# Kernel tuning notes

Hardware: AMD Instinct MI355X
Metric: run time of the kernel (lower is better)

The kernel has to match this reference:

```python
import jax, jax.numpy as jnp
import numpy as np
import math

DIM, DEPTH, HEADS, DH, MLP = 512, 12, 8, 64, 2048
EPS = 1e-5

def _ln(x, g, b):
    m = jnp.mean(x, -1, keepdims=True)
    v = jnp.var(x, -1, keepdims=True)
    return (x - m) * jax.lax.rsqrt(v + EPS) * g + b

def _gelu(x):
    return jax.nn.gelu(x, approximate=False)  # torch nn.GELU default = exact erf

def _conv1d(x, w, b):
    # x: [B, Cin, T], w: [Cout, Cin, 7], 'same' padding
    y = jax.lax.conv_general_dilated(x, w, (1,), [(3, 3)], dimension_numbers=('NCH', 'OIH', 'NCH'))
    return y + b[None, :, None]

def setup_inputs() -> dict:
    key = jax.random.key(0)
    ks = iter(jax.random.split(key, 64))
    def w(shape, s=0.02):
        return jax.random.normal(next(ks), shape, jnp.float32) * s
    return {
        'x': jax.random.normal(next(ks), (2, 1024), jnp.float32),
        'timesteps': jax.random.uniform(next(ks), (2,), jnp.float32) * 1000.0,
        'cond': jax.random.normal(next(ks), (2, 64, DIM), jnp.float32),
        'conv_w1': w((DIM // 2, 1, 7)), 'conv_b1': jnp.zeros((DIM // 2,), jnp.float32),
        'conv_w2': w((DIM, DIM // 2, 7)), 'conv_b2': jnp.zeros((DIM,), jnp.float32),
        'tpe_w1': w((DIM, 4 * DIM)), 'tpe_b1': jnp.zeros((4 * DIM,), jnp.float32),
        'tpe_w2': w((4 * DIM, DIM)), 'tpe_b2': jnp.zeros((DIM,), jnp.float32),
        'ln1_g': jnp.ones((DEPTH, DIM), jnp.float32), 'ln1_b': jnp.zeros((DEPTH, DIM), jnp.float32),
        'wq': w((DEPTH, DIM, HEADS * DH)), 'wkv': w((DEPTH, DIM, 2 * DH)),
        'wo': w((DEPTH, HEADS * DH, DIM)), 'bo': jnp.zeros((DEPTH, DIM), jnp.float32),
        'ln2_g': jnp.ones((DEPTH, DIM), jnp.float32), 'ln2_b': jnp.zeros((DEPTH, DIM), jnp.float32),
        'ffn_w1': w((DEPTH, DIM, MLP)), 'ffn_b1': jnp.zeros((DEPTH, MLP), jnp.float32),
        'ffn_w2': w((DEPTH, MLP, DIM)), 'ffn_b2': jnp.zeros((DEPTH, DIM), jnp.float32),
        'tm_w1': w((DEPTH, DIM, 4 * DIM)), 'tm_b1': jnp.zeros((DEPTH, 4 * DIM), jnp.float32),
        'tm_w2': w((DEPTH, 4 * DIM, DIM)), 'tm_b2': jnp.zeros((DEPTH, DIM), jnp.float32),
        'fn_g': jnp.ones((DIM,), jnp.float32), 'fn_b': jnp.zeros((DIM,), jnp.float32),
        'out_w1': w((DIM, 2 * DIM)), 'out_b1': jnp.zeros((2 * DIM,), jnp.float32),
        'out_w2': w((2 * DIM, 1)), 'out_b2': jnp.zeros((1,), jnp.float32),
    }

def reference(x, timesteps, cond, conv_w1, conv_b1, conv_w2, conv_b2,
              tpe_w1, tpe_b1, tpe_w2, tpe_b2,
              ln1_g, ln1_b, wq, wkv, wo, bo, ln2_g, ln2_b,
              ffn_w1, ffn_b1, ffn_w2, ffn_b2, tm_w1, tm_b1, tm_w2, tm_b2,
              fn_g, fn_b, out_w1, out_b1, out_w2, out_b2):
    b, T = x.shape
    # audio encoder: conv -> relu -> conv -> relu
    h = _conv1d(x[:, None, :], conv_w1, conv_b1)
    h = jax.nn.relu(h)
    h = _conv1d(h, conv_w2, conv_b2)
    h = jax.nn.relu(h)
    h = h.transpose(0, 2, 1)  # [b, T, dim]
    # sinusoidal time embedding + MLP
    half = DIM // 2
    freqs = jnp.exp(jnp.arange(half, dtype=jnp.float32) * (-math.log(10000.0) / (half - 1)))
    te = timesteps[:, None] * freqs[None, :]
    te = jnp.concatenate([jnp.sin(te), jnp.cos(te)], axis=-1)  # [b, dim]
    time_emb = _gelu(te @ tpe_w1 + tpe_b1) @ tpe_w2 + tpe_b2
    # concat text conditioning tokens
    h = jnp.concatenate([h, cond], axis=1)  # [b, n, dim]
    bsz, n, _ = h.shape
    scale = DH ** -0.5

    def block(hx, p):
        g1, b1, Wq, Wkv, Wo, Bo, g2, b2, F1, Fb1, F2, Fb2, T1, Tb1, T2, Tb2 = p
        tm = _gelu(time_emb @ T1 + Tb1) @ T2 + Tb2  # [b, dim]
        hx = _ln(hx, g1, b1)
        q = (hx @ Wq).reshape(bsz, n, HEADS, DH).transpose(0, 2, 1, 3)  # [b,h,n,d]
        kv = hx @ Wkv
        k, v = kv[..., :DH], kv[..., DH:]  # shared single KV head [b,n,d]
        dots = jnp.einsum('bhnd,bmd->bhnm', q, k) * scale
        attn = jax.nn.softmax(dots, axis=-1)
        o = jnp.einsum('bhnm,bmd->bhnd', attn, v)
        o = o.transpose(0, 2, 1, 3).reshape(bsz, n, HEADS * DH) @ Wo + Bo
        hx = hx + o
        hx = hx + tm[:, None, :]
        hx = _ln(hx, g2, b2)
        hx = hx + (_gelu(hx @ F1 + Fb1) @ F2 + Fb2)
        return hx, None

    h, _ = jax.lax.scan(block, h, (ln1_g, ln1_b, wq, wkv, wo, bo, ln2_g, ln2_b,
                                   ffn_w1, ffn_b1, ffn_w2, ffn_b2,
                                   tm_w1, tm_b1, tm_w2, tm_b2))
    h = _ln(h, fn_g, fn_b)
    h = _gelu(h @ out_w1 + out_b1) @ out_w2 + out_b2  # [b, n, 1]
    return h[:, :T, 0]
```

## Files before the change

kernel.cpp:

```cpp
#include <hip/hip_runtime.h>
#include <hip/hip_bf16.h>
#include <math.h>


typedef unsigned short u16;
typedef __attribute__((ext_vector_type(8))) short short8;
typedef __attribute__((ext_vector_type(8))) unsigned short ushort8;
typedef __attribute__((ext_vector_type(4))) float f32x4;

#define MFMA_B16(a, b, c) __builtin_amdgcn_mfma_f32_16x16x32_bf16(a, b, c, 0, 0, 0)

__device__ __forceinline__ float gelu_f(float x) {
  return 0.5f * x * (1.f + erff(x * 0.70710678118654752f));
}
__device__ __forceinline__ u16 f2b(float x) {
  union { float f; unsigned u; } v;
  v.f = x;
  unsigned r = (v.u + 0x7FFF + ((v.u >> 16) & 1)) >> 16;
  return (u16)r;
}
__device__ __forceinline__ float b2f(u16 u) {
  union { unsigned u; float f; } v;
  v.u = ((unsigned)u) << 16;
  return v.f;
}

#define MODE_BIAS 1
#define MODE_GELU 2
#define MODE_RES 4
#define MODE_TM 8
#define MODE_OUT16 16
#define MODE_KVT 32
#define MODE_RELU 64
#define MODE_CONVROW 128

__global__ void te_k(const float* __restrict__ ts, float* __restrict__ te) {
  int t = threadIdx.x;
  int b = t >> 8, i = t & 255;
  float tv = ts[b];
  float fr = __expf((float)i * (-9.210340371976184f / 255.f));
  float arg = tv * fr;
  te[b * 512 + i] = sinf(arg);
  te[b * 512 + 256 + i] = cosf(arg);
}

__global__ __launch_bounds__(256) void mlpA_k(const float* __restrict__ A,
                                              const float* __restrict__ B,
                                              float* __restrict__ part, int K,
                                              int N, long sA, long sB) {
  int l = blockIdx.z;
  const float* Ap = A + (size_t)l * sA;
  const float* Bp = B + (size_t)l * sB;
  int KS = K >> 7;
  int tid = threadIdx.x;
  int c16 = tid & 15;
  int col = blockIdx.x * 64 + c16 * 4;
  int kr = tid >> 4;
  int k0 = blockIdx.y * 128 + kr;
  float4 a0 = {0.f, 0.f, 0.f, 0.f}, a1 = {0.f, 0.f, 0.f, 0.f};
#pragma unroll
  for (int i = 0; i < 8; ++i) {
    int k = k0 + i * 16;
    float4 bv = *(const float4*)&Bp[(size_t)k * N + col];
    float x0 = Ap[k], x1 = Ap[K + k];
    a0.x = fmaf(x0, bv.x, a0.x);
    a0.y = fmaf(x0, bv.y, a0.y);
    a0.z = fmaf(x0, bv.z, a0.z);
    a0.w = fmaf(x0, bv.w, a0.w);
    a1.x = fmaf(x1, bv.x, a1.x);
    a1.y = fmaf(x1, bv.y, a1.y);
    a1.z = fmaf(x1, bv.z, a1.z);
    a1.w = fmaf(x1, bv.w, a1.w);
  }
#pragma unroll
  for (int off = 16; off < 64; off <<= 1) {
    a0.x += __shfl_xor(a0.x, off);
    a0.y += __shfl_xor(a0.y, off);
    a0.z += __shfl_xor(a0.z, off);
    a0.w += __shfl_xor(a0.w, off);
    a1.x += __shfl_xor(a1.x, off);
    a1.y += __shfl_xor(a1.y, off);
    a1.z += __shfl_xor(a1.z, off);
    a1.w += __shfl_xor(a1.w, off);
  }
  __shared__ float red[4][2][64];
  int w = tid >> 6, lane = tid & 63;
  if (lane < 16) {
    *(float4*)&red[w][0][c16 * 4] = a0;
    *(float4*)&red[w][1][c16 * 4] = a1;
  }
  __syncthreads();
  if (tid < 128) {
    int m = tid >> 6, c = tid & 63;
    float s = red[0][m][c] + red[1][m][c] + red[2][m][c] + red[3][m][c];
    part[(((size_t)l * KS + blockIdx.y) * 2 + m) * N + blockIdx.x * 64 + c] = s;
  }
}

__global__ __launch_bounds__(256) void mlpB_k(const float* __restrict__ part,
                                              const float* __restrict__ bias,
                                              float* __restrict__ C, int N,
                                              int lgN, int KS, int dogelu,
                                              long sb, long sC) {
  int idx = blockIdx.x * 256 + threadIdx.x;
  int col = idx & (N - 1);
  int lm = idx >> lgN;
  int m = lm & 1, l = lm >> 1;
  float s = 0.f;
  for (int ks = 0; ks < KS; ++ks)
    s += part[(((size_t)l * KS + ks) * 2 + m) * N + col];
  s += bias[(size_t)l * sb + col];
  if (dogelu) s = gelu_f(s);
  C[(size_t)l * sC + (size_t)m * N + col] = s;
}

__global__ __launch_bounds__(256) void conv1_k(const float* __restrict__ x,
                                               const float* __restrict__ w1,
                                               const float* __restrict__ b1,
                                               float* __restrict__ buf1) {
  int idx = blockIdx.x * 256 + threadIdx.x;
  int t = idx & 1023, co = (idx >> 10) & 255, b = idx >> 18;
  float acc = b1[co];
#pragma unroll
  for (int k = 0; k < 7; ++k) {
    int gt = t + k - 3;
    if (gt >= 0 && gt < 1024)
      acc = fmaf(w1[co * 7 + k], x[b * 1024 + gt], acc);
  }
  buf1[idx] = fmaxf(acc, 0.f);
}

__global__ __launch_bounds__(256) void im2col_k(const float* __restrict__ buf1,
                                                u16* __restrict__ A16) {
  int idx = blockIdx.x * 256 + threadIdx.x;
  int c = idx % 1792;
  int m = idx / 1792;
  int b = m >> 10, tt = m & 1023;
  int ci = c / 7, k = c - ci * 7;
  int gt = tt + k - 3;
  float v = (gt >= 0 && gt < 1024) ? buf1[((b * 256) + ci) * 1024 + gt] : 0.f;
  A16[idx] = f2b(v);
}

__global__ void cond_k(const float* __restrict__ cond,
                       float* __restrict__ hbuf) {
  int idx = blockIdx.x * 256 + threadIdx.x;
  int b = idx >> 15, rem = idx & 32767;
  int j = rem >> 9, cc = rem & 511;
  hbuf[(size_t)(b * 1088 + 1024 + j) * 512 + cc] = cond[idx];
}

__global__ __launch_bounds__(256) void ln_k(float* __restrict__ h,
                                            u16* __restrict__ h16,
                                            const float* __restrict__ g,
                                            const float* __restrict__ bb) {
  int row = blockIdx.x;
  float* p = h + (size_t)row * 512;
  int t = threadIdx.x;
  float x0 = p[t], x1 = p[t + 256];
  float s = x0 + x1, q = x0 * x0 + x1 * x1;
#pragma unroll
  for (int off = 1; off < 64; off <<= 1) {
    s += __shfl_xor(s, off);
    q += __shfl_xor(q, off);
  }
  __shared__ float ps[4], pq[4];
  int w = t >> 6, lane = t & 63;
  if (lane == 0) {
    ps[w] = s;
    pq[w] = q;
  }
  __syncthreads();
  s = ps[0] + ps[1] + ps[2] + ps[3];
  q = pq[0] + pq[1] + pq[2] + pq[3];
  float mean = s * (1.f / 512.f);
  float var = q * (1.f / 512.f) - mean * mean;
  float rs = rsqrtf(var + 1e-5f);
  float v0 = (x0 - mean) * rs * g[t] + bb[t];
  float v1 = (x1 - mean) * rs * g[t + 256] + bb[t + 256];
  p[t] = v0;
  p[t + 256] = v1;
  h16[(size_t)row * 512 + t] = f2b(v0);
  h16[(size_t)row * 512 + t + 256] = f2b(v1);
}

__device__ __forceinline__ void wcvt_tile(float (*T)[65],
                                          const float* __restrict__ src,
                                          u16* __restrict__ dst, int K, int N,
                                          int tk, int tn, int t) {
  int kl = t >> 2, nseg = (t & 3) * 16;
#pragma unroll
  for (int j = 0; j < 4; ++j) {
    float4 v =
        *(const float4*)&src[(size_t)(tk * 64 + kl) * N + tn * 64 + nseg + j * 4];
    T[nseg + j * 4 + 0][kl] = v.x;
    T[nseg + j * 4 + 1][kl] = v.y;
    T[nseg + j * 4 + 2][kl] = v.z;
    T[nseg + j * 4 + 3][kl] = v.w;
  }
  __syncthreads();
  int nl = t >> 2, kseg = (t & 3) * 16;
#pragma unroll
  for (int j = 0; j < 4; ++j) {
    ushort4 o;
    o.x = f2b(T[nl][kseg + j * 4 + 0]);
    o.y = f2b(T[nl][kseg + j * 4 + 1]);
    o.z = f2b(T[nl][kseg + j * 4 + 2]);
    o.w = f2b(T[nl][kseg + j * 4 + 3]);
    *(ushort4*)&dst[(size_t)(tn * 64 + nl) * K + tk * 64 + kseg + j * 4] = o;
  }
}

__global__ __launch_bounds__(256) void wcvt5_k(
    const float* wq, const float* wkv, const float* wo, const float* w1,
    const float* w2, u16* dq, u16* dkv, u16* dwo, u16* d1, u16* d2) {
  __shared__ float T[64][65];
  int bid = blockIdx.x, t = threadIdx.x;
  if (bid < 64) {
    wcvt_tile(T, wq, dq, 512, 512, bid >> 3, bid & 7, t);
  } else if (bid < 80) {
    int id = bid - 64;
    wcvt_tile(T, wkv, dkv, 512, 128, id >> 1, id & 1, t);
  } else if (bid < 144) {
    int id = bid - 80;
    wcvt_tile(T, wo, dwo, 512, 512, id >> 3, id & 7, t);
  } else if (bid < 400) {
    int id = bid - 144;
    wcvt_tile(T, w1, d1, 512, 2048, id >> 5, id & 31, t);
  } else {
    int id = bid - 400;
    wcvt_tile(T, w2, d2, 2048, 512, id >> 3, id & 7, t);
  }
}

__global__ __launch_bounds__(256) void wcvtT_k(const float* src, u16* dst,
                                               int K, int N) {
  __shared__ float T[64][65];
  int nt = N >> 6;
  int tk = blockIdx.x / nt, tn = blockIdx.x % nt;
  wcvt_tile(T, src, dst, K, N, tk, tn, threadIdx.x);
}

__global__ __launch_bounds__(256) void fcvt_k(const float* __restrict__ src,
                                              u16* __restrict__ dst, int n) {
  int i = (blockIdx.x * 256 + threadIdx.x) * 4;
  if (i >= n) return;
  float4 v = *(const float4*)&src[i];
  ushort4 o;
  o.x = f2b(v.x);
  o.y = f2b(v.y);
  o.z = f2b(v.z);
  o.w = f2b(v.w);
  *(ushort4*)&dst[i] = o;
}

__global__ __launch_bounds__(256) void bgemm2_k(
    const u16* __restrict__ A, const u16* __restrict__ B,
    const float* __restrict__ bias, const float* __restrict__ tmv,
    const float* __restrict__ res, float* __restrict__ Cf,
    u16* __restrict__ C16, u16* __restrict__ C16b, float* __restrict__ part,
    int K, int N, int Kblk, int MN, int mode) {
  __shared__ u16 As[2][64 * 72];
  __shared__ u16 Bs[2][64 * 72];
  int t = threadIdx.x;
  int n0 = blockIdx.x * 64, m0 = blockIdx.y * 64;
  int kz = blockIdx.z;
  int wid = t >> 6, lane = t & 63;
  int quad = lane >> 4, l15 = lane & 15;
  int wr = (wid >> 1) * 32, wc = (wid & 1) * 32;
  int sr = t >> 2, sc = (t & 3) * 16;
  const u16* Ap = A + (size_t)(m0 + sr) * K + (size_t)kz * Kblk + sc;
  const u16* Bp = B + (size_t)(n0 + sr) * K + (size_t)kz * Kblk + sc;

  f32x4 acc[2][2];
#pragma unroll
  for (int i = 0; i < 2; ++i)
#pragma unroll
    for (int j = 0; j < 2; ++j) acc[i][j] = (f32x4){0.f, 0.f, 0.f, 0.f};

  int nt = Kblk >> 6;
  ushort8 ra0 = *(const ushort8*)Ap;
  ushort8 ra1 = *(const ushort8*)(Ap + 8);
  ushort8 rb0 = *(const ushort8*)Bp;
  ushort8 rb1 = *(const ushort8*)(Bp + 8);
  *(ushort8*)&As[0][sr * 72 + sc] = ra0;
  *(ushort8*)&As[0][sr * 72 + sc + 8] = ra1;
  *(ushort8*)&Bs[0][sr * 72 + sc] = rb0;
  *(ushort8*)&Bs[0][sr * 72 + sc + 8] = rb1;
  __syncthreads();
  int cur = 0;
  for (int tt = 0; tt < nt; ++tt) {
    if (tt + 1 < nt) {
      const u16* ap = Ap + (tt + 1) * 64;
      const u16* bp = Bp + (tt + 1) * 64;
      ra0 = *(const ushort8*)ap;
      ra1 = *(const ushort8*)(ap + 8);
      rb0 = *(const ushort8*)bp;
      rb1 = *(const ushort8*)(bp + 8);
    }
    short8 af[2][2], bf[2][2];
#pragma unroll
    for (int s = 0; s < 2; ++s)
#pragma unroll
      for (int i = 0; i < 2; ++i) {
        af[i][s] =
            *(const short8*)&As[cur][(wr + i * 16 + l15) * 72 + s * 32 + quad * 8];
        bf[i][s] =
            *(const short8*)&Bs[cur][(wc + i * 16 + l15) * 72 + s * 32 + quad * 8];
      }
#pragma unroll
    for (int s = 0; s < 2; ++s)
#pragma unroll
      for (int i = 0; i < 2; ++i)
#pragma unroll
        for (int j = 0; j < 2; ++j)
          acc[i][j] = MFMA_B16(af[i][s], bf[j][s], acc[i][j]);
    if (tt + 1 < nt) {
      int nx = cur ^ 1;
      *(ushort8*)&As[nx][sr * 72 + sc] = ra0;
      *(ushort8*)&As[nx][sr * 72 + sc + 8] = ra1;
      *(ushort8*)&Bs[nx][sr * 72 + sc] = rb0;
      *(ushort8*)&Bs[nx][sr * 72 + sc + 8] = rb1;
      __syncthreads();
      cur = nx;
    }
  }

  if (gridDim.z > 1) {
#pragma unroll
    for (int i = 0; i < 2; ++i)
#pragma unroll
      for (int reg = 0; reg < 4; ++reg) {
        int row = m0 + wr + i * 16 + quad * 4 + reg;
#pragma unroll
        for (int j = 0; j < 2; ++j) {
          int col = n0 + wc + j * 16 + l15;
          part[(size_t)kz * MN + (size_t)row * N + col] = acc[i][j][reg];
        }
      }
    return;
  }

#pragma unroll
  for (int i = 0; i < 2; ++i) {
#pragma unroll
    for (int reg = 0; reg < 4; ++reg) {
      int row = m0 + wr + i * 16 + quad * 4 + reg;
      int orow = (mode & MODE_CONVROW) ? row + ((row >> 10) << 6) : row;
#pragma unroll
      for (int j = 0; j < 2; ++j) {
        int col = n0 + wc + j * 16 + l15;
        float v = acc[i][j][reg];
        if (mode & MODE_BIAS) v += bias[col];
        if (mode & MODE_TM) v += tmv[(row >= 1088 ? 512 : 0) + col];
        if (mode & MODE_RES) v += res[(size_t)orow * 512 + col];
        if (mode & MODE_GELU) v = gelu_f(v);
        if (mode & MODE_RELU) v = fmaxf(v, 0.f);
        if (mode & MODE_KVT) {
          if (col < 64)
            C16[orow * 64 + col] = f2b(v);
          else
            C16b[(size_t)(col - 64) * 2176 + orow] = f2b(v);
        } else if (mode & MODE_OUT16) {
          C16[(size_t)orow * N + col] = f2b(v);
        } else {
          Cf[(size_t)orow * N + col] = v;
        }
      }
    }
  }
}

__global__ __launch_bounds__(256) void bred_k(
    const float* __restrict__ part, const float* __restrict__ bias,
    const float* __restrict__ tmv, const float* __restrict__ res,
    float* __restrict__ Cf, u16* __restrict__ C16, u16* __restrict__ C16b,
    int MN, int Nmask, int lgN, int S, int mode) {
  int idx = (blockIdx.x * 256 + threadIdx.x) * 4;
  if (idx >= MN) return;
  int row = idx >> lgN;
  int col = idx & Nmask;
  float4 s = *(const float4*)&part[idx];
  for (int ss = 1; ss < S; ++ss) {
    float4 p = *(const float4*)&part[(size_t)ss * MN + idx];
    s.x += p.x;
    s.y += p.y;
    s.z += p.z;
    s.w += p.w;
  }
  float v[4] = {s.x, s.y, s.z, s.w};
#pragma unroll
  for (int j = 0; j < 4; ++j) {
    float vv = v[j];
    int c = col + j;
    if (mode & MODE_BIAS) vv += bias[c];
    if (mode & MODE_TM) vv += tmv[(row >= 1088 ? 512 : 0) + c];
    if (mode & MODE_RES) vv += res[(size_t)row * 512 + c];
    if (mode & MODE_GELU) vv = gelu_f(vv);
    v[j] = vv;
  }
  if (mode & MODE_KVT) {
    if (col < 64) {
      ushort4 o;
      o.x = f2b(v[0]);
      o.y = f2b(v[1]);
      o.z = f2b(v[2]);
      o.w = f2b(v[3]);
      *(ushort4*)&C16[row * 64 + col] = o;
    } else {
#pragma unroll
      for (int j = 0; j < 4; ++j)
        C16b[(size_t)(col - 64 + j) * 2176 + row] = f2b(v[j]);
    }
  } else if (mode & MODE_OUT16) {
    ushort4 o;
    o.x = f2b(v[0]);
    o.y = f2b(v[1]);
    o.z = f2b(v[2]);
    o.w = f2b(v[3]);
    *(ushort4*)&C16[idx] = o;
  } else {
    float4 o = {v[0], v[1], v[2], v[3]};
    *(float4*)&Cf[idx] = o;
  }
}

__global__ __launch_bounds__(256) void attn2_k(const u16* __restrict__ q,
                                               const u16* __restrict__ k16,
                                               const u16* __restrict__ vT16,
                                               u16* __restrict__ opart,
                                               float* __restrict__ ml) {
  __shared__ u16 Qs[64 * 72];
  __shared__ u16 Ks[2][64 * 72];
  __shared__ u16 VT[2][64 * 72];
  __shared__ u16 Ps[64 * 72];
  int t = threadIdx.x;
  int qt = blockIdx.x, h = blockIdx.y;
  int b = blockIdx.z >> 1, s = blockIdx.z & 1;
  int kt0 = s * 9;
  int ktn = 9 - s;
  int wid = t >> 6, lane = t & 63;
  int quad = lane >> 4, l15 = lane & 15;
  int w16 = wid * 16;
  int r = t >> 2, seg = (t & 3) * 16;
  {
    const u16* qp = q + (size_t)(b * 1088 + qt * 64 + r) * 512 + h * 64 + seg;
    *(ushort8*)&Qs[r * 72 + seg] = *(const ushort8*)qp;
    *(ushort8*)&Qs[r * 72 + seg + 8] = *(const ushort8*)(qp + 8);
  }
  const u16* kbase = k16 + (size_t)(b * 1088 + kt0 * 64 + r) * 64 + seg;
  const u16* vbase = vT16 + (size_t)r * 2176 + b * 1088 + kt0 * 64 + seg;
  *(ushort8*)&Ks[0][r * 72 + seg] = *(const ushort8*)kbase;
  *(ushort8*)&Ks[0][r * 72 + seg + 8] = *(const ushort8*)(kbase + 8);
  *(ushort8*)&VT[0][r * 72 + seg] = *(const ushort8*)vbase;
  *(ushort8*)&VT[0][r * 72 + seg + 8] = *(const ushort8*)(vbase + 8);
  __syncthreads();

  f32x4 accO[4];
#pragma unroll
  for (int i = 0; i < 4; ++i) accO[i] = (f32x4){0.f, 0.f, 0.f, 0.f};
  float mi[4] = {-1e30f, -1e30f, -1e30f, -1e30f};
  float li[4] = {0.f, 0.f, 0.f, 0.f};

  int cur = 0;
  ushort8 rk0, rk1, rv0, rv1;
  for (int kt = 0; kt < ktn; ++kt) {
    if (kt + 1 < ktn) {
      const u16* kp = kbase + (size_t)(kt + 1) * 64 * 64;
      const u16* vp = vbase + (kt + 1) * 64;
      rk0 = *(const ushort8*)kp;
      rk1 = *(const ushort8*)(kp + 8);
      rv0 = *(const ushort8*)vp;
      rv1 = *(const ushort8*)(vp + 8);
    }
    f32x4 sc[4];
#pragma unroll
    for (int sn = 0; sn < 4; ++sn) sc[sn] = (f32x4){0.f, 0.f, 0.f, 0.f};
#pragma unroll
    for (int ss = 0; ss < 2; ++ss) {
      short8 a = *(const short8*)&Qs[(w16 + l15) * 72 + ss * 32 + quad * 8];
#pragma unroll
      for (int sn = 0; sn < 4; ++sn) {
        short8 bb =
            *(const short8*)&Ks[cur][(sn * 16 + l15) * 72 + ss * 32 + quad * 8];
        sc[sn] = MFMA_B16(a, bb, sc[sn]);
      }
    }
#pragma unroll
    for (int reg = 0; reg < 4; ++reg) {
      float s0 = sc[0][reg] * 0.125f, s1 = sc[1][reg] * 0.125f;
      float s2 = sc[2][reg] * 0.125f, s3 = sc[3][reg] * 0.125f;
      float mx = fmaxf(fmaxf(s0, s1), fmaxf(s2, s3));
#pragma unroll
      for (int off = 1; off < 16; off <<= 1) mx = fmaxf(mx, __shfl_xor(mx, off));
      float mn = fmaxf(mi[reg], mx);
      float al = __expf(mi[reg] - mn);
      mi[reg] = mn;
      float p0 = __expf(s0 - mn), p1 = __expf(s1 - mn);
      float p2 = __expf(s2 - mn), p3 = __expf(s3 - mn);
      int rr = (w16 + quad * 4 + reg) * 72 + l15;
      Ps[rr] = f2b(p0);
      Ps[rr + 16] = f2b(p1);
      Ps[rr + 32] = f2b(p2);
      Ps[rr + 48] = f2b(p3);
      float psum = p0 + p1 + p2 + p3;
#pragma unroll
      for (int off = 1; off < 16; off <<= 1) psum += __shfl_xor(psum, off);
      li[reg] = li[reg] * al + psum;
#pragma unroll
      for (int sn = 0; sn < 4; ++sn) accO[sn][reg] *= al;
    }
#pragma unroll
    for (int ss = 0; ss < 2; ++ss) {
      short8 pa = *(const short8*)&Ps[(w16 + l15) * 72 + ss * 32 + quad * 8];
#pragma unroll
      for (int sn = 0; sn < 4; ++sn) {
        short8 vb =
            *(const short8*)&VT[cur][(sn * 16 + l15) * 72 + ss * 32 + quad * 8];
        accO[sn] = MFMA_B16(pa, vb, accO[sn]);
      }
    }
    if (kt + 1 < ktn) {
      int nx = cur ^ 1;
      *(ushort8*)&Ks[nx][r * 72 + seg] = rk0;
      *(ushort8*)&Ks[nx][r * 72 + seg + 8] = rk1;
      *(ushort8*)&VT[nx][r * 72 + seg] = rv0;
      *(ushort8*)&VT[nx][r * 72 + seg + 8] = rv1;
      __syncthreads();
      cur = nx;
    }
  }
  size_t pbase = (((size_t)(s * 2 + b) * 8 + h) * 1088 + qt * 64);
#pragma unroll
  for (int reg = 0; reg < 4; ++reg) {
    float inv = 1.f / li[reg];
    int rr = w16 + quad * 4 + reg;
#pragma unroll
    for (int sn = 0; sn < 4; ++sn) {
      opart[(pbase + rr) * 64 + sn * 16 + l15] = f2b(accO[sn][reg] * inv);
    }
    if (l15 == 0) {
      ml[(pbase + rr) * 2] = mi[reg];
      ml[(pbase + rr) * 2 + 1] = li[reg];
    }
  }
}

__global__ __launch_bounds__(256) void amerge_k(const u16* __restrict__ opart,
                                                const float* __restrict__ ml,
                                                u16* __restrict__ o) {
  int idx = blockIdx.x * 256 + threadIdx.x;
  int d4 = (idx & 15) * 4;
  int rem = idx >> 4;
  int row = rem % 1088;
  int bh = rem / 1088;
  int h = bh & 7, b = bh >> 3;
  size_t r0 = ((size_t)(0 + b) * 8 + h) * 1088 + row;
  size_t r1 = ((size_t)(2 + b) * 8 + h) * 1088 + row;
  float m0 = ml[r0 * 2], l0 = ml[r0 * 2 + 1];
  float m1 = ml[r1 * 2], l1 = ml[r1 * 2 + 1];
  float m = fmaxf(m0, m1);
  float w0 = l0 * __expf(m0 - m), w1 = l1 * __expf(m1 - m);
  float inv = 1.f / (w0 + w1);
  w0 *= inv;
  w1 *= inv;
  ushort4 a = *(const ushort4*)&opart[r0 * 64 + d4];
  ushort4 c = *(const ushort4*)&opart[r1 * 64 + d4];
  ushort4 ov;
  ov.x = f2b(w0 * b2f(a.x) + w1 * b2f(c.x));
  ov.y = f2b(w0 * b2f(a.y) + w1 * b2f(c.y));
  ov.z = f2b(w0 * b2f(a.z) + w1 * b2f(c.z));
  ov.w = f2b(w0 * b2f(a.w) + w1 * b2f(c.w));
  *(ushort4*)&o[(size_t)(b * 1088 + row) * 512 + h * 64 + d4] = ov;
}

__global__ __launch_bounds__(256) void outvec_k(const u16* __restrict__ G,
                                               const float* __restrict__ w,
                                               const float* __restrict__ b2,
                                               float* __restrict__ out) {
  int row = blockIdx.x;
  int b = row >> 10, tt = row & 1023;
  const u16* g = G + (size_t)(b * 1088 + tt) * 1024;
  int k0 = threadIdx.x * 4;
  ushort4 gv = *(const ushort4*)&g[k0];
  float acc = b2f(gv.x) * w[k0] + b2f(gv.y) * w[k0 + 1] +
              b2f(gv.z) * w[k0 + 2] + b2f(gv.w) * w[k0 + 3];
#pragma unroll
  for (int off = 1; off < 64; off <<= 1) acc += __shfl_xor(acc, off);
  __shared__ float part[4];
  int wv = threadIdx.x >> 6, lane = threadIdx.x & 63;
  if (lane == 0) part[wv] = acc;
  __syncthreads();
  if (threadIdx.x == 0) {
    out[row] = part[0] + part[1] + part[2] + part[3] + b2[0];
  }
}

extern "C" void kernel_launch(void* const* d_in, const int* in_sizes, int n_in,
                              void* d_out, int out_size, void* d_ws,
                              size_t ws_size, hipStream_t stream) {
  (void)in_sizes;
  (void)n_in;
  (void)out_size;
  const float* x = (const float*)d_in[0];
  const float* timesteps = (const float*)d_in[1];
  const float* cond = (const float*)d_in[2];
  const float* conv_w1 = (const float*)d_in[3];
  const float* conv_b1 = (const float*)d_in[4];
  const float* conv_w2 = (const float*)d_in[5];
  const float* conv_b2 = (const float*)d_in[6];
  const float* tpe_w1 = (const float*)d_in[7];
  const float* tpe_b1 = (const float*)d_in[8];
  const float* tpe_w2 = (const float*)d_in[9];
  const float* tpe_b2 = (const float*)d_in[10];
  const float* ln1_g = (const float*)d_in[11];
  const float* ln1_b = (const float*)d_in[12];
  const float* wq = (const float*)d_in[13];
  const float* wkv = (const float*)d_in[14];
  const float* wo = (const float*)d_in[15];
  const float* bo = (const float*)d_in[16];
  const float* ln2_g = (const float*)d_in[17];
  const float* ln2_b = (const float*)d_in[18];
  const float* ffn_w1 = (const float*)d_in[19];
  const float* ffn_b1 = (const float*)d_in[20];
  const float* ffn_w2 = (const float*)d_in[21];
  const float* ffn_b2 = (const float*)d_in[22];
  const float* tm_w1 = (const float*)d_in[23];
  const float* tm_b1 = (const float*)d_in[24];
  const float* tm_w2 = (const float*)d_in[25];
  const float* tm_b2 = (const float*)d_in[26];
  const float* fn_g = (const float*)d_in[27];
  const float* fn_b = (const float*)d_in[28];
  const float* out_w1 = (const float*)d_in[29];
  const float* out_b1 = (const float*)d_in[30];
  const float* out_w2 = (const float*)d_in[31];
  const float* out_b2 = (const float*)d_in[32];

  float* w = (float*)d_ws;
  float* te = w + 0;
  float* tpe_mid = w + 1024;
  float* time_emb = w + 5120;
  float* tm_mid = w + 6144;
  float* tm = w + 55296;
  float* hbuf = w + 131072;
  u16* q16 = (u16*)(w + 1245184);
  float* buf1 = w + 1245184;
  u16* hb16 = (u16*)(w + 1802240);
  u16* k16 = (u16*)(w + 2359296);
  u16* vT16 = (u16*)(w + 2428928);
  u16* mid16 = (u16*)(w + 2498560);
  u16* im16 = mid16;
  u16* g16 = mid16;
  u16* wbuf = (u16*)(w + 4726784);
  u16* wq16 = wbuf;
  u16* wkv16 = wbuf + 262144;
  u16* wo16 = wbuf + 327680;
  u16* w116 = wbuf + 589824;
  u16* w216 = wbuf + 1638400;
  u16* cw216 = wbuf;
  u16* ow116 = wbuf;
  float* pmlp = hbuf;
  float* pmid = w + 2498560;
  u16* opart16 = (u16*)(w + 2498560);
  float* aml = w + 2498560 + 1114112;
  int big = ws_size >= (size_t)(6070272 + 2228224) * 4 ? 1 : 0;
  float* part2 = w + 6070272;

  te_k<<<1, 512, 0, stream>>>(timesteps, te);
  mlpA_k<<<dim3(32, 4, 1), 256, 0, stream>>>(te, tpe_w1, pmlp, 512, 2048, 0, 0);
  mlpB_k<<<16, 256, 0, stream>>>(pmlp, tpe_b1, tpe_mid, 2048, 11, 4, 1, 0, 0);
  mlpA_k<<<dim3(8, 16, 1), 256, 0, stream>>>(tpe_mid, tpe_w2, pmlp, 2048, 512,
                                             0, 0);
  mlpB_k<<<4, 256, 0, stream>>>(pmlp, tpe_b2, time_emb, 512, 9, 16, 0, 0, 0);
  mlpA_k<<<dim3(32, 4, 12), 256, 0, stream>>>(time_emb, tm_w1, pmlp, 512, 2048,
                                              0, 512L * 2048);
  mlpB_k<<<192, 256, 0, stream>>>(pmlp, tm_b1, tm_mid, 2048, 11, 4, 1, 2048,
                                  2L * 2048);
  mlpA_k<<<dim3(8, 16, 12), 256, 0, stream>>>(tm_mid, tm_w2, pmlp, 2048, 512,
                                              2L * 2048, 2048L * 512);
  mlpB_k<<<48, 256, 0, stream>>>(pmlp, tm_b2, tm, 512, 9, 16, 0, 512,
                                 2L * 512);

  conv1_k<<<2048, 256, 0, stream>>>(x, conv_w1, conv_b1, buf1);
  fcvt_k<<<896, 256, 0, stream>>>(conv_w2, cw216, 917504);
  im2col_k<<<14336, 256, 0, stream>>>(buf1, im16);
  bgemm2_k<<<dim3(8, 32, 1), 256, 0, stream>>>(
      im16, cw216, conv_b2, nullptr, nullptr, hbuf, nullptr, nullptr, nullptr,
      1792, 512, 1792, 0, MODE_BIAS | MODE_RELU | MODE_CONVROW);
  cond_k<<<256, 256, 0, stream>>>(cond, hbuf);

  for (int l = 0; l < 12; ++l) {
    wcvt5_k<<<656, 256, 0, stream>>>(
        wq + (size_t)l * 512 * 512, wkv + (size_t)l * 512 * 128,
        wo + (size_t)l * 512 * 512, ffn_w1 + (size_t)l * 512 * 2048,
        ffn_w2 + (size_t)l * 2048 * 512, wq16, wkv16, wo16, w116, w216);
    ln_k<<<2176, 256, 0, stream>>>(hbuf, hb16, ln1_g + l * 512,
                                   ln1_b + l * 512);
    bgemm2_k<<<dim3(8, 34, 2), 256, 0, stream>>>(
        hb16, wq16, nullptr, nullptr, nullptr, nullptr, nullptr, nullptr,
        pmid, 512, 512, 256, 1114112, 0);
    bred_k<<<1088, 256, 0, stream>>>(pmid, nullptr, nullptr, nullptr, nullptr,
                                     q16, nullptr, 1114112, 511, 9, 2,
                                     MODE_OUT16);
    bgemm2_k<<<dim3(2, 34, 2), 256, 0, stream>>>(
        hb16, wkv16, nullptr, nullptr, nullptr, nullptr, nullptr, nullptr,
        pmid, 512, 128, 256, 278528, 0);
    bred_k<<<272, 256, 0, stream>>>(pmid, nullptr, nullptr, nullptr, nullptr,
                                    k16, vT16, 278528, 127, 7, 2, MODE_KVT);
    attn2_k<<<dim3(17, 8, 4), 256, 0, stream>>>(q16, k16, vT16, opart16, aml);
    amerge_k<<<1088, 256, 0, stream>>>(opart16, aml, q16);
    bgemm2_k<<<dim3(8, 34, 2), 256, 0, stream>>>(
        q16, wo16, nullptr, nullptr, nullptr, nullptr, nullptr, nullptr, pmid,
        512, 512, 256, 1114112, 0);
    bred_k<<<1088, 256, 0, stream>>>(pmid, bo + l * 512, tm + l * 1024, hbuf,
                                     hbuf, nullptr, nullptr, 1114112, 511, 9,
                                     2, MODE_BIAS | MODE_TM | MODE_RES);
    ln_k<<<2176, 256, 0, stream>>>(hbuf, hb16, ln2_g + l * 512,
                                   ln2_b + l * 512);
    bgemm2_k<<<dim3(32, 34, 1), 256, 0, stream>>>(
        hb16, w116, ffn_b1 + l * 2048, nullptr, nullptr, nullptr, mid16,
        nullptr, nullptr, 512, 2048, 512, 0,
        MODE_BIAS | MODE_GELU | MODE_OUT16);
    if (big) {
      bgemm2_k<<<dim3(8, 34, 2), 256, 0, stream>>>(
          mid16, w216, nullptr, nullptr, nullptr, nullptr, nullptr, nullptr,
          part2, 2048, 512, 1024, 1114112, 0);
      bred_k<<<1088, 256, 0, stream>>>(part2, ffn_b2 + l * 512, nullptr, hbuf,
                                       hbuf, nullptr, nullptr, 1114112, 511, 9,
                                       2, MODE_BIAS | MODE_RES);
    } else {
      bgemm2_k<<<dim3(8, 34, 1), 256, 0, stream>>>(
          mid16, w216, ffn_b2 + l * 512, nullptr, hbuf, hbuf, nullptr,
          nullptr, nullptr, 2048, 512, 2048, 0, MODE_BIAS | MODE_RES);
    }
  }
  ln_k<<<2176, 256, 0, stream>>>(hbuf, hb16, fn_g, fn_b);
  wcvtT_k<<<128, 256, 0, stream>>>(out_w1, ow116, 512, 1024);
  bgemm2_k<<<dim3(16, 34, 1), 256, 0, stream>>>(
      hb16, ow116, out_b1, nullptr, nullptr, nullptr, g16, nullptr, nullptr,
      512, 1024, 512, 0, MODE_BIAS | MODE_GELU | MODE_OUT16);
  outvec_k<<<2048, 256, 0, stream>>>(g16, out_w2, out_b2, (float*)d_out);
}
```

Baseline: 1.860 ms.

## Fuse QKV GEMM, LN into residual reduce, batch weight conversion, 4-way attention split

When the workspace is large enough, all 12 layers' weights are converted to bf16 in one batched launch instead of once per layer. Q and KV projections become a single N=640 GEMM whose reduce kernel scatters q, k and vT. The split-K reduce after Wo and after FFN2 now also applies LayerNorm, which removes the separate ln_k passes. Attention splits the key range four ways instead of two for more parallelism, at the cost of a larger merge and a new path that runs only above a workspace-size threshold.

```diff
diff --git a/kernel.cpp b/kernel.cpp
--- a/kernel.cpp
+++ b/kernel.cpp
@@ -33,6 +33,7 @@
 #define MODE_KVT 32
 #define MODE_RELU 64
 #define MODE_CONVROW 128
+#define MODE_QKV 256
 
 __global__ void te_k(const float* __restrict__ ts, float* __restrict__ te) {
   int t = threadIdx.x;
@@ -211,11 +212,11 @@
   }
 }
 
-__global__ __launch_bounds__(256) void wcvt5_k(
-    const float* wq, const float* wkv, const float* wo, const float* w1,
-    const float* w2, u16* dq, u16* dkv, u16* dwo, u16* d1, u16* d2) {
-  __shared__ float T[64][65];
-  int bid = blockIdx.x, t = threadIdx.x;
+__device__ __forceinline__ void wcvt5_body(const float* wq, const float* wkv,
+                                           const float* wo, const float* w1,
+                                           const float* w2, u16* dq, u16* dkv,
+                                           u16* dwo, u16* d1, u16* d2,
+                                           float (*T)[65], int bid, int t) {
   if (bid < 64) {
     wcvt_tile(T, wq, dq, 512, 512, bid >> 3, bid & 7, t);
   } else if (bid < 80) {
@@ -231,6 +232,26 @@
     int id = bid - 400;
     wcvt_tile(T, w2, d2, 2048, 512, id >> 3, id & 7, t);
   }
+}
+
+__global__ __launch_bounds__(256) void wcvt5_k(
+    const float* wq, const float* wkv, const float* wo, const float* w1,
+    const float* w2, u16* dq, u16* dkv, u16* dwo, u16* d1, u16* d2) {
+  __shared__ float T[64][65];
+  wcvt5_body(wq, wkv, wo, w1, w2, dq, dkv, dwo, d1, d2, T, blockIdx.x,
+             threadIdx.x);
+}
+
+__global__ __launch_bounds__(256) void wcvt5b_k(
+    const float* wq, const float* wkv, const float* wo, const float* w1,
+    const float* w2, u16* wall) {
+  __shared__ float T[64][65];
+  int l = blockIdx.y;
+  u16* d = wall + (size_t)l * 2686976;
+  wcvt5_body(wq + (size_t)l * 262144, wkv + (size_t)l * 65536,
+             wo + (size_t)l * 262144, w1 + (size_t)l * 1048576,
+             w2 + (size_t)l * 1048576, d, d + 262144, d + 327680, d + 589824,
+             d + 1638400, T, blockIdx.x, threadIdx.x);
 }
 
 __global__ __launch_bounds__(256) void wcvtT_k(const float* src, u16* dst,
@@ -375,11 +396,11 @@
     const float* __restrict__ part, const float* __restrict__ bias,
     const float* __restrict__ tmv, const float* __restrict__ res,
     float* __restrict__ Cf, u16* __restrict__ C16, u16* __restrict__ C16b,
-    int MN, int Nmask, int lgN, int S, int mode) {
+    u16* __restrict__ C16c, int MN, int N, int S, int mode) {
   int idx = (blockIdx.x * 256 + threadIdx.x) * 4;
   if (idx >= MN) return;
-  int row = idx >> lgN;
-  int col = idx & Nmask;
+  int row = idx / N;
+  int col = idx - row * N;
   float4 s = *(const float4*)&part[idx];
   for (int ss = 1; ss < S; ++ss) {
     float4 p = *(const float4*)&part[(size_t)ss * MN + idx];
@@ -399,7 +420,27 @@
     if (mode & MODE_GELU) vv = gelu_f(vv);
     v[j] = vv;
   }
-  if (mode & MODE_KVT) {
+  if (mode & MODE_QKV) {
+    if (col < 512) {
+      ushort4 o;
+      o.x = f2b(v[0]);
+      o.y = f2b(v[1]);
+      o.z = f2b(v[2]);
+      o.w = f2b(v[3]);
+      *(ushort4*)&C16[(size_t)row * 512 + col] = o;
+    } else if (col < 576) {
+      ushort4 o;
+      o.x = f2b(v[0]);
+      o.y = f2b(v[1]);
+      o.z = f2b(v[2]);
+      o.w = f2b(v[3]);
+      *(ushort4*)&C16b[row * 64 + (col - 512)] = o;
+    } else {
+#pragma unroll
+      for (int j = 0; j < 4; ++j)
+        C16c[(size_t)(col - 576 + j) * 2176 + row] = f2b(v[j]);
+    }
+  } else if (mode & MODE_KVT) {
     if (col < 64) {
       ushort4 o;
       o.x = f2b(v[0]);
@@ -425,20 +466,75 @@
   }
 }
 
+__global__ __launch_bounds__(256) void bredln_k(
+    const float* __restrict__ part, const float* __restrict__ bias,
+    const float* __restrict__ tmv, float* __restrict__ hbuf,
+    u16* __restrict__ h16, const float* __restrict__ g,
+    const float* __restrict__ bb, int S, int mode) {
+  int row = blockIdx.x;
+  int t = threadIdx.x;
+  size_t base = (size_t)row * 512;
+  float v0 = part[base + t], v1 = part[base + t + 256];
+  for (int ss = 1; ss < S; ++ss) {
+    v0 += part[(size_t)ss * 1114112 + base + t];
+    v1 += part[(size_t)ss * 1114112 + base + t + 256];
+  }
+  if (mode & MODE_BIAS) {
+    v0 += bias[t];
+    v1 += bias[t + 256];
+  }
+  if (mode & MODE_TM) {
+    int off = (row >= 1088) ? 512 : 0;
+    v0 += tmv[off + t];
+    v1 += tmv[off + t + 256];
+  }
+  if (mode & MODE_RES) {
+    v0 += hbuf[base + t];
+    v1 += hbuf[base + t + 256];
+  }
+  float s = v0 + v1, q = v0 * v0 + v1 * v1;
+#pragma unroll
+  for (int off = 1; off < 64; off <<= 1) {
+    s += __shfl_xor(s, off);
+    q += __shfl_xor(q, off);
+  }
+  __shared__ float ps[4], pq[4];
+  int w = t >> 6, lane = t & 63;
+  if (lane == 0) {
+    ps[w] = s;
+    pq[w] = q;
+  }
+  __syncthreads();
+  s = ps[0] + ps[1] + ps[2] + ps[3];
+  q = pq[0] + pq[1] + pq[2] + pq[3];
+  float mean = s * (1.f / 512.f);
+  float var = q * (1.f / 512.f) - mean * mean;
+  float rs = rsqrtf(var + 1e-5f);
+  float n0 = (v0 - mean) * rs * g[t] + bb[t];
+  float n1 = (v1 - mean) * rs * g[t + 256] + bb[t + 256];
+  hbuf[base + t] = n0;
+  hbuf[base + t + 256] = n1;
+  h16[base + t] = f2b(n0);
+  h16[base + t + 256] = f2b(n1);
+}
+
 __global__ __launch_bounds__(256) void attn2_k(const u16* __restrict__ q,
                                                const u16* __restrict__ k16,
                                                const u16* __restrict__ vT16,
                                                u16* __restrict__ opart,
-                                               float* __restrict__ ml) {
+                                               float* __restrict__ ml,
+                                               int nsplit) {
   __shared__ u16 Qs[64 * 72];
   __shared__ u16 Ks[2][64 * 72];
   __shared__ u16 VT[2][64 * 72];
   __shared__ u16 Ps[64 * 72];
   int t = threadIdx.x;
   int qt = blockIdx.x, h = blockIdx.y;
-  int b = blockIdx.z >> 1, s = blockIdx.z & 1;
-  int kt0 = s * 9;
-  int ktn = 9 - s;
+  int zz = blockIdx.z;
+  int s = zz % nsplit, b = zz / nsplit;
+  int tbase = 17 / nsplit, trem = 17 % nsplit;
+  int kt0 = s * tbase + (s < trem ? s : trem);
+  int ktn = tbase + (s < trem ? 1 : 0);
   int wid = t >> 6, lane = t & 63;
   int quad = lane >> 4, l15 = lane & 15;
   int w16 = wid * 16;
@@ -548,29 +644,35 @@
 
 __global__ __launch_bounds__(256) void amerge_k(const u16* __restrict__ opart,
                                                 const float* __restrict__ ml,
-                                                u16* __restrict__ o) {
+                                                u16* __restrict__ o, int S) {
   int idx = blockIdx.x * 256 + threadIdx.x;
   int d4 = (idx & 15) * 4;
   int rem = idx >> 4;
   int row = rem % 1088;
   int bh = rem / 1088;
   int h = bh & 7, b = bh >> 3;
-  size_t r0 = ((size_t)(0 + b) * 8 + h) * 1088 + row;
-  size_t r1 = ((size_t)(2 + b) * 8 + h) * 1088 + row;
-  float m0 = ml[r0 * 2], l0 = ml[r0 * 2 + 1];
-  float m1 = ml[r1 * 2], l1 = ml[r1 * 2 + 1];
-  float m = fmaxf(m0, m1);
-  float w0 = l0 * __expf(m0 - m), w1 = l1 * __expf(m1 - m);
-  float inv = 1.f / (w0 + w1);
-  w0 *= inv;
-  w1 *= inv;
-  ushort4 a = *(const ushort4*)&opart[r0 * 64 + d4];
-  ushort4 c = *(const ushort4*)&opart[r1 * 64 + d4];
+  float m = -1e30f;
+  for (int s = 0; s < S; ++s) {
+    size_t rs = ((size_t)(s * 2 + b) * 8 + h) * 1088 + row;
+    m = fmaxf(m, ml[rs * 2]);
+  }
+  float a0 = 0.f, a1 = 0.f, a2 = 0.f, a3 = 0.f, wsum = 0.f;
+  for (int s = 0; s < S; ++s) {
+    size_t rs = ((size_t)(s * 2 + b) * 8 + h) * 1088 + row;
+    float wgt = ml[rs * 2 + 1] * __expf(ml[rs * 2] - m);
+    wsum += wgt;
+    ushort4 a = *(const ushort4*)&opart[rs * 64 + d4];
+    a0 += wgt * b2f(a.x);
+    a1 += wgt * b2f(a.y);
+    a2 += wgt * b2f(a.z);
+    a3 += wgt * b2f(a.w);
+  }
+  float inv = 1.f / wsum;
   ushort4 ov;
-  ov.x = f2b(w0 * b2f(a.x) + w1 * b2f(c.x));
-  ov.y = f2b(w0 * b2f(a.y) + w1 * b2f(c.y));
-  ov.z = f2b(w0 * b2f(a.z) + w1 * b2f(c.z));
-  ov.w = f2b(w0 * b2f(a.w) + w1 * b2f(c.w));
+  ov.x = f2b(a0 * inv);
+  ov.y = f2b(a1 * inv);
+  ov.z = f2b(a2 * inv);
+  ov.w = f2b(a3 * inv);
   *(ushort4*)&o[(size_t)(b * 1088 + row) * 512 + h * 64 + d4] = ov;
 }
 
@@ -661,10 +763,13 @@
   u16* ow116 = wbuf;
   float* pmlp = hbuf;
   float* pmid = w + 2498560;
-  u16* opart16 = (u16*)(w + 2498560);
-  float* aml = w + 2498560 + 1114112;
+  float* part2 = w + 6070272;
+  float* pqkv = w + 8298496;
+  float* amlh = w + 11083776;
+  u16* wall = (u16*)(w + 11362304);
+  u16* opart16h = (u16*)(w + 2498560);
   int big = ws_size >= (size_t)(6070272 + 2228224) * 4 ? 1 : 0;
-  float* part2 = w + 6070272;
+  int huge = ws_size >= (size_t)120 * 1024 * 1024 ? 1 : 0;
 
   te_k<<<1, 512, 0, stream>>>(timesteps, te);
   mlpA_k<<<dim3(32, 4, 1), 256, 0, stream>>>(te, tpe_w1, pmlp, 512, 2048, 0, 0);
@@ -689,6 +794,51 @@
       1792, 512, 1792, 0, MODE_BIAS | MODE_RELU | MODE_CONVROW);
   cond_k<<<256, 256, 0, stream>>>(cond, hbuf);
 
+  if (huge) {
+    wcvt5b_k<<<dim3(656, 12), 256, 0, stream>>>(wq, wkv, wo, ffn_w1, ffn_w2,
+                                                wall);
+    ln_k<<<2176, 256, 0, stream>>>(hbuf, hb16, ln1_g, ln1_b);
+    for (int l = 0; l < 12; ++l) {
+      u16* uW = wall + (size_t)l * 2686976;
+      bgemm2_k<<<dim3(10, 34, 2), 256, 0, stream>>>(
+          hb16, uW, nullptr, nullptr, nullptr, nullptr, nullptr, nullptr,
+          pqkv, 512, 640, 256, 1392640, 0);
+      bred_k<<<1360, 256, 0, stream>>>(pqkv, nullptr, nullptr, nullptr,
+                                       nullptr, q16, k16, vT16, 1392640, 640,
+                                       2, MODE_QKV);
+      attn2_k<<<dim3(17, 8, 8), 256, 0, stream>>>(q16, k16, vT16, opart16h,
+                                                  amlh, 4);
+      amerge_k<<<1088, 256, 0, stream>>>(opart16h, amlh, q16, 4);
+      bgemm2_k<<<dim3(8, 34, 2), 256, 0, stream>>>(
+          q16, uW + 327680, nullptr, nullptr, nullptr, nullptr, nullptr,
+          nullptr, pmid, 512, 512, 256, 1114112, 0);
+      bredln_k<<<2176, 256, 0, stream>>>(pmid, bo + l * 512, tm + l * 1024,
+                                         hbuf, hb16, ln2_g + l * 512,
+                                         ln2_b + l * 512, 2,
+                                         MODE_BIAS | MODE_TM | MODE_RES);
+      bgemm2_k<<<dim3(32, 34, 1), 256, 0, stream>>>(
+          hb16, uW + 589824, ffn_b1 + l * 2048, nullptr, nullptr, nullptr,
+          mid16, nullptr, nullptr, 512, 2048, 512, 0,
+          MODE_BIAS | MODE_GELU | MODE_OUT16);
+      bgemm2_k<<<dim3(8, 34, 2), 256, 0, stream>>>(
+          mid16, uW + 1638400, nullptr, nullptr, nullptr, nullptr, nullptr,
+          nullptr, part2, 2048, 512, 1024, 1114112, 0);
+      const float* gp = (l == 11) ? fn_g : ln1_g + (l + 1) * 512;
+      const float* bp = (l == 11) ? fn_b : ln1_b + (l + 1) * 512;
+      bredln_k<<<2176, 256, 0, stream>>>(part2, ffn_b2 + l * 512, nullptr,
+                                         hbuf, hb16, gp, bp, 2,
+                                         MODE_BIAS | MODE_RES);
+    }
+    wcvtT_k<<<128, 256, 0, stream>>>(out_w1, ow116, 512, 1024);
+    bgemm2_k<<<dim3(16, 34, 1), 256, 0, stream>>>(
+        hb16, ow116, out_b1, nullptr, nullptr, nullptr, g16, nullptr, nullptr,
+        512, 1024, 512, 0, MODE_BIAS | MODE_GELU | MODE_OUT16);
+    outvec_k<<<2048, 256, 0, stream>>>(g16, out_w2, out_b2, (float*)d_out);
+    return;
+  }
+
+  u16* opart16 = (u16*)(w + 2498560);
+  float* aml = w + 2498560 + 1114112;
   for (int l = 0; l < 12; ++l) {
     wcvt5_k<<<656, 256, 0, stream>>>(
         wq + (size_t)l * 512 * 512, wkv + (size_t)l * 512 * 128,
@@ -700,21 +850,23 @@
         hb16, wq16, nullptr, nullptr, nullptr, nullptr, nullptr, nullptr,
         pmid, 512, 512, 256, 1114112, 0);
     bred_k<<<1088, 256, 0, stream>>>(pmid, nullptr, nullptr, nullptr, nullptr,
-                                     q16, nullptr, 1114112, 511, 9, 2,
+                                     q16, nullptr, nullptr, 1114112, 512, 2,
                                      MODE_OUT16);
     bgemm2_k<<<dim3(2, 34, 2), 256, 0, stream>>>(
         hb16, wkv16, nullptr, nullptr, nullptr, nullptr, nullptr, nullptr,
         pmid, 512, 128, 256, 278528, 0);
     bred_k<<<272, 256, 0, stream>>>(pmid, nullptr, nullptr, nullptr, nullptr,
-                                    k16, vT16, 278528, 127, 7, 2, MODE_KVT);
-    attn2_k<<<dim3(17, 8, 4), 256, 0, stream>>>(q16, k16, vT16, opart16, aml);
-    amerge_k<<<1088, 256, 0, stream>>>(opart16, aml, q16);
+                                    k16, vT16, nullptr, 278528, 128, 2,
+                                    MODE_KVT);
+    attn2_k<<<dim3(17, 8, 4), 256, 0, stream>>>(q16, k16, vT16, opart16, aml,
+                                                2);
+    amerge_k<<<1088, 256, 0, stream>>>(opart16, aml, q16, 2);
     bgemm2_k<<<dim3(8, 34, 2), 256, 0, stream>>>(
         q16, wo16, nullptr, nullptr, nullptr, nullptr, nullptr, nullptr, pmid,
         512, 512, 256, 1114112, 0);
     bred_k<<<1088, 256, 0, stream>>>(pmid, bo + l * 512, tm + l * 1024, hbuf,
-                                     hbuf, nullptr, nullptr, 1114112, 511, 9,
-                                     2, MODE_BIAS | MODE_TM | MODE_RES);
+                                     hbuf, nullptr, nullptr, nullptr, 1114112,
+                                     512, 2, MODE_BIAS | MODE_TM | MODE_RES);
     ln_k<<<2176, 256, 0, stream>>>(hbuf, hb16, ln2_g + l * 512,
                                    ln2_b + l * 512);
     bgemm2_k<<<dim3(32, 34, 1), 256, 0, stream>>>(
@@ -726,8 +878,8 @@
           mid16, w216, nullptr, nullptr, nullptr, nullptr, nullptr, nullptr,
           part2, 2048, 512, 1024, 1114112, 0);
       bred_k<<<1088, 256, 0, stream>>>(part2, ffn_b2 + l * 512, nullptr, hbuf,
-                                       hbuf, nullptr, nullptr, 1114112, 511, 9,
-                                       2, MODE_BIAS | MODE_RES);
+                                       hbuf, nullptr, nullptr, nullptr,
+                                       1114112, 512, 2, MODE_BIAS | MODE_RES);
     } else {
       bgemm2_k<<<dim3(8, 34, 1), 256, 0, stream>>>(
           mid16, w216, ffn_b2 + l * 512, nullptr, hbuf, hbuf, nullptr,
```

Result: faster. 1.646 ms (-11.5%).
